# Kernel tuning notes

Measured on AMD Instinct MI355X. Metric: run time of the kernel, lower is better.

## Reference

```python
import jax, jax.numpy as jnp
import numpy as np

N, E, M = 4096, 65536, 16   # nodes, edges, channel multiplicity per degree
MID = 32                    # RadialFunc hidden width (SE3-Transformer default)
EPS = 1e-5                  # BatchNorm1d eps
DEGS = [0, 1]
PAIRS = [(0, 0), (0, 1), (1, 0), (1, 1)]  # (d_in, d_out)


def _bn_relu(x, g, b):
    # BatchNorm1d in training mode (biased batch stats over edges) + ReLU
    mu = x.mean(0, keepdims=True)
    var = ((x - mu) ** 2).mean(0, keepdims=True)
    return jax.nn.relu((x - mu) / jnp.sqrt(var + EPS) * g + b)


def _radial(feat, w1, b1, g1, be1, w2, b2, g2, be2, w3, b3, nf):
    # RadialFunc: Linear-BN-ReLU, Linear-BN-ReLU, Linear -> [E, nc_out, 1, nc_in, 1, nf]
    y = _bn_relu(feat @ w1 + b1, g1, be1)
    y = _bn_relu(y @ w2 + b2, g2, be2)
    y = y @ w3 + b3
    return y.reshape(-1, M, 1, M, 1, nf)


def _forward(h0, h1, r, basis00, basis01, basis10, basis11,
             rw1, rb1, rg1, rbe1, rw2, rb2, rg2, rbe2,
             w3_00, b3_00, w3_01, b3_01, w3_10, b3_10, w3_11, b3_11,
             Wself0, Wself1, edge_src, edge_dst):
    h = {0: h0, 1: h1}
    basis = {(0, 0): basis00, (0, 1): basis01, (1, 0): basis10, (1, 1): basis11}
    w3b3 = {(0, 0): (w3_00, b3_00), (0, 1): (w3_01, b3_01),
            (1, 0): (w3_10, b3_10), (1, 1): (w3_11, b3_11)}
    Wself = {0: Wself0, 1: Wself1}
    # PairwiseConv: per-edge kernel = sum_f R * basis  -> [E, M, 2do+1, M, 2di+1]
    kern = {}
    for p, (di, do) in enumerate(PAIRS):
        nf = 2 * min(di, do) + 1
        w3, b3 = w3b3[(di, do)]
        R = _radial(r, rw1[p], rb1[p], rg1[p], rbe1[p],
                    rw2[p], rb2[p], rg2[p], rbe2[p], w3, b3, nf)
        kern[(di, do)] = (R * basis[(di, do)]).sum(-1)
    cnt = jnp.maximum(
        jax.ops.segment_sum(jnp.ones((E,), h0.dtype), edge_dst, num_segments=N), 1.0)
    outs = []
    for do in DEGS:
        msg = jnp.zeros((E, M, 2 * do + 1), h0.dtype)
        for di in DEGS:
            # per-edge small matmul: kernel @ gathered source feature
            msg = msg + jnp.einsum('eopiq,eiq->eop', kern[(di, do)], h[di][edge_src])
        # self-interaction, flavor='skip': add W @ destination feature per edge
        msg = msg + jnp.einsum('mi,eip->emp', Wself[do][0], h[do][edge_dst])
        s = jax.ops.segment_sum(msg, edge_dst, num_segments=N)  # scatter-mean
        outs.append(s / cnt[:, None, None])
    return tuple(outs)


def setup_inputs() -> dict:
    key = jax.random.key(0)
    ks = jax.random.split(key, 20)
    nrm = lambda k, sh, s=1.0: jax.random.normal(k, sh, jnp.float32) * s
    return {
        'h0': nrm(ks[0], (N, M, 1)),
        'h1': nrm(ks[1], (N, M, 3)),
        'r': jax.random.uniform(ks[2], (E, 1), jnp.float32),
        'basis00': nrm(ks[3], (E, 1, 1, 1, 1, 1)),
        'basis01': nrm(ks[4], (E, 1, 3, 1, 1, 1)),
        'basis10': nrm(ks[5], (E, 1, 1, 1, 3, 1)),
        'basis11': nrm(ks[6], (E, 1, 3, 1, 3, 3)),
        'rw1': nrm(ks[7], (4, 1, MID)),
        'rb1': jnp.zeros((4, MID), jnp.float32),
        'rg1': jnp.ones((4, MID), jnp.float32),
        'rbe1': jnp.zeros((4, MID), jnp.float32),
        'rw2': nrm(ks[8], (4, MID, MID), 1.0 / np.sqrt(MID)),
        'rb2': jnp.zeros((4, MID), jnp.float32),
        'rg2': jnp.ones((4, MID), jnp.float32),
        'rbe2': jnp.zeros((4, MID), jnp.float32),
        'w3_00': nrm(ks[9], (MID, M * M), 1.0 / np.sqrt(MID)),
        'b3_00': jnp.zeros((M * M,), jnp.float32),
        'w3_01': nrm(ks[10], (MID, M * M), 1.0 / np.sqrt(MID)),
        'b3_01': jnp.zeros((M * M,), jnp.float32),
        'w3_10': nrm(ks[11], (MID, M * M), 1.0 / np.sqrt(MID)),
        'b3_10': jnp.zeros((M * M,), jnp.float32),
        'w3_11': nrm(ks[12], (MID, M * M * 3), 1.0 / np.sqrt(MID)),
        'b3_11': jnp.zeros((M * M * 3,), jnp.float32),
        'Wself0': nrm(ks[13], (1, M, M), 1.0 / np.sqrt(M)),
        'Wself1': nrm(ks[14], (1, M, M), 1.0 / np.sqrt(M)),
        'edge_src': jax.random.randint(ks[15], (E,), 0, N),
        'edge_dst': jax.random.randint(ks[16], (E,), 0, N),
    }


def reference(h0, h1, r, basis00, basis01, basis10, basis11,
              rw1, rb1, rg1, rbe1, rw2, rb2, rg2, rbe2,
              w3_00, b3_00, w3_01, b3_01, w3_10, b3_10, w3_11, b3_11,
              Wself0, Wself1, edge_src, edge_dst):
    return _forward(h0, h1, r, basis00, basis01, basis10, basis11,
                    rw1, rb1, rg1, rbe1, rw2, rb2, rg2, rbe2,
                    w3_00, b3_00, w3_01, b3_01, w3_10, b3_10, w3_11, b3_11,
                    Wself0, Wself1, edge_src, edge_dst)
```

## Files before the change

kernel.cpp:

```cpp
#include <hip/hip_runtime.h>

#define N_NODES 4096
#define N_EDGES 65536
#define MID 32
#define BN_EPS 1e-5f

#define WS_RSUM    0
#define WS_RSUMSQ  1
#define WS_ALPHA1  272
#define WS_BETA1   400
#define WS_A2      528
#define WS_S2      656
#define WS_GRAM    5120
#define WS_SUMY    9216
#define WS_W2T     17664
#define WS_MSG_F   262144
#define WS_U00     4456448
#define WS_U01     4521984
#define WS_V10     4587520
#define WS_W11     4784128
#define WS_DEG_I   1024
#define WS_CUR_I   9344
#define WS_OFFS_I  13440
#define WS_ELIST_I 65536
#define WSB_WA     524288
#define WSB_WB     557056
#define WSB_WC     573440

typedef short bf16x8 __attribute__((ext_vector_type(8)));
typedef float f32x4  __attribute__((ext_vector_type(4)));

__device__ __forceinline__ unsigned short f2bf(float x) {
    unsigned u = __float_as_uint(x);
    u += 0x7fffu + ((u >> 16) & 1u);
    return (unsigned short)(u >> 16);
}

__global__ void __launch_bounds__(256) k_pre(const float* __restrict__ rw2,
        const float* __restrict__ w300, const float* __restrict__ w301,
        const float* __restrict__ w310, const float* __restrict__ w311,
        const float* __restrict__ bw300, const float* __restrict__ bw301,
        const float* __restrict__ bw310, const float* __restrict__ bw311,
        const float* __restrict__ r, const int* __restrict__ edst,
        const float* __restrict__ h0, const float* __restrict__ h1,
        float* __restrict__ wsf) {
    if (blockIdx.x < 128) {
        int t = blockIdx.x * 256 + threadIdx.x;
        char* wsb = (char*)wsf;
        if (t < 4096) {
            int p = t >> 10, rem = t & 1023, c = rem >> 5, k = rem & 31;
            wsf[WS_W2T + t] = rw2[(p << 10) + (k << 5) + c];
        }
        if (t < 16384) {
            int col = t >> 5, k = t & 31;
            float v = (col < 256) ? w300[(k << 8) + col] : w310[(k << 8) + (col - 256)];
            ((unsigned short*)(wsb + WSB_WA))[t] = f2bf(v);
        }
        if (t < 8192) {
            int col = t >> 5, k = t & 31;
            ((unsigned short*)(wsb + WSB_WB))[t] = f2bf(w301[(k << 8) + col]);
        }
        if (t < 24576) {
            int col = t >> 5, k = t & 31;
            int f = col >> 8, rem = col & 255;
            ((unsigned short*)(wsb + WSB_WC))[t] = f2bf(w311[k * 768 + rem * 3 + f]);
        }
    } else if (blockIdx.x < 384) {
        int e = (blockIdx.x - 128) * 256 + threadIdx.x;
        float v = r[e];
        atomicAdd(((int*)wsf) + WS_DEG_I + edst[e], 1);
        float s = v, ss = v * v;
#pragma unroll
        for (int mk = 32; mk >= 1; mk >>= 1) {
            s  += __shfl_xor(s,  mk, 64);
            ss += __shfl_xor(ss, mk, 64);
        }
        __shared__ float ls[4], lss[4];
        int lane = threadIdx.x & 63, wv = threadIdx.x >> 6;
        if (lane == 0) { ls[wv] = s; lss[wv] = ss; }
        __syncthreads();
        if (threadIdx.x == 0) {
            atomicAdd(wsf + WS_RSUM,   ls[0] + ls[1] + ls[2] + ls[3]);
            atomicAdd(wsf + WS_RSUMSQ, lss[0] + lss[1] + lss[2] + lss[3]);
        }
    } else {
        int g = (blockIdx.x - 384) * 256 + threadIdx.x;
        int n = g >> 4, mo = g & 15;
        float s00 = 0.f, s01 = 0.f;
#pragma unroll
        for (int mi = 0; mi < 16; ++mi) {
            float hv = h0[n * 16 + mi];
            s00 += bw300[mo * 16 + mi] * hv;
            s01 += bw301[mo * 16 + mi] * hv;
        }
        wsf[WS_U00 + n * 16 + mo] = s00;
        wsf[WS_U01 + n * 16 + mo] = s01;
#pragma unroll
        for (int q = 0; q < 3; ++q) {
            float sv = 0.f;
#pragma unroll
            for (int mi = 0; mi < 16; ++mi)
                sv += bw310[mo * 16 + mi] * h1[n * 48 + mi * 3 + q];
            wsf[WS_V10 + n * 48 + q * 16 + mo] = sv;
        }
#pragma unroll 1
        for (int f = 0; f < 3; ++f)
#pragma unroll 1
            for (int q = 0; q < 3; ++q) {
                float sv = 0.f;
#pragma unroll
                for (int mi = 0; mi < 16; ++mi)
                    sv += bw311[(mo * 16 + mi) * 3 + f] * h1[n * 48 + mi * 3 + q];
                wsf[WS_W11 + n * 144 + (f * 3 + q) * 16 + mo] = sv;
            }
    }
}

__global__ void __launch_bounds__(512) k_gram(const float* __restrict__ r,
        const float* __restrict__ rw1, const float* __restrict__ rg1,
        const float* __restrict__ rbe1, float* __restrict__ wsf) {
    int t = threadIdx.x;
    int wv = t >> 6, lane = t & 63;
    int quad = lane >> 4, lq = lane & 15;
    int p  = __builtin_amdgcn_readfirstlane(wv & 3);
    int mt = __builtin_amdgcn_readfirstlane(wv >> 2);
    float mu_r  = wsf[WS_RSUM] * (1.f / N_EDGES);
    float var_r = wsf[WS_RSUMSQ] * (1.f / N_EDGES) - mu_r * mu_r;
    float al[2], be[2];
#pragma unroll
    for (int hh = 0; hh < 2; ++hh) {
        int ch = p * 32 + hh * 16 + lq;
        float w1 = rw1[ch];
        float a = w1 * rg1[ch] * rsqrtf(w1 * w1 * var_r + BN_EPS);
        al[hh] = a;
        be[hh] = rbe1[ch] - a * mu_r;
    }
    bf16x8 ones;
#pragma unroll
    for (int j = 0; j < 8; ++j) ones[j] = (short)0x3F80;
    f32x4 accG0 = {0.f, 0.f, 0.f, 0.f};
    f32x4 accG1 = {0.f, 0.f, 0.f, 0.f};
    f32x4 accS  = {0.f, 0.f, 0.f, 0.f};
    int ebase = blockIdx.x * 512;
#pragma unroll 1
    for (int ks = 0; ks < 16; ++ks) {
        const float* rp = r + ebase + ks * 32 + quad * 8;
        float4 ra = *(const float4*)(rp);
        float4 rb = *(const float4*)(rp + 4);
        float rv[8] = {ra.x, ra.y, ra.z, ra.w, rb.x, rb.y, rb.z, rb.w};
        bf16x8 fr0, fr1;
#pragma unroll
        for (int j = 0; j < 8; ++j) {
            fr0[j] = (short)f2bf(fmaxf(0.f, al[0] * rv[j] + be[0]));
            fr1[j] = (short)f2bf(fmaxf(0.f, al[1] * rv[j] + be[1]));
        }
        bf16x8 fA = mt ? fr1 : fr0;
        accG0 = __builtin_amdgcn_mfma_f32_16x16x32_bf16(fA, fr0, accG0, 0, 0, 0);
        accG1 = __builtin_amdgcn_mfma_f32_16x16x32_bf16(fA, fr1, accG1, 0, 0, 0);
        accS  = __builtin_amdgcn_mfma_f32_16x16x32_bf16(fA, ones, accS,  0, 0, 0);
    }
    float* G = wsf + WS_GRAM + p * 1024;
#pragma unroll
    for (int reg = 0; reg < 4; ++reg) {
        int k1 = mt * 16 + quad * 4 + reg;
        atomicAdd(&G[k1 * 32 + lq],      accG0[reg]);
        atomicAdd(&G[k1 * 32 + 16 + lq], accG1[reg]);
    }
    if (lq == 0) {
#pragma unroll
        for (int reg = 0; reg < 4; ++reg)
            atomicAdd(wsf + WS_SUMY + p * 32 + mt * 16 + quad * 4 + reg, accS[reg]);
    }
}

__global__ void __launch_bounds__(1024) k_fs(const float* __restrict__ rw1,
        const float* __restrict__ rg1, const float* __restrict__ rbe1,
        const float* __restrict__ rg2, const float* __restrict__ rbe2,
        const float* __restrict__ rb2, float* __restrict__ wsf) {
    int t = threadIdx.x;
    if (t < 128) {
        float mu_r  = wsf[WS_RSUM] * (1.f / N_EDGES);
        float var_r = wsf[WS_RSUMSQ] * (1.f / N_EDGES) - mu_r * mu_r;
        float w1 = rw1[t];
        float al = w1 * rg1[t] * rsqrtf(w1 * w1 * var_r + BN_EPS);
        wsf[WS_ALPHA1 + t] = al;
        wsf[WS_BETA1  + t] = rbe1[t] - al * mu_r;
        int p = t >> 5, c = t & 31;
        const float* G = wsf + WS_GRAM + p * 1024;
        const float* w = wsf + WS_W2T + p * 1024 + c * 32;
        float invE = 1.f / N_EDGES;
        float s1 = 0.f;
#pragma unroll 1
        for (int k = 0; k < 32; ++k) s1 += w[k] * (wsf[WS_SUMY + p * 32 + k] * invE);
        float q = 0.f;
#pragma unroll 1
        for (int k1 = 0; k1 < 32; ++k1) {
            float a = 0.f;
#pragma unroll
            for (int k2 = 0; k2 < 32; ++k2) a += w[k2] * G[k1 * 32 + k2];
            q += w[k1] * a;
        }
        float var = q * invE - s1 * s1;
        float a2 = rg2[t] * rsqrtf(var + BN_EPS);
        wsf[WS_A2 + t] = a2;
        float mu2 = rb2[t] + s1;
        wsf[WS_S2 + t] = rbe2[t] - mu2 * a2;
    }
    __shared__ int sdata[1024];
    const int* deg = ((const int*)wsf) + WS_DEG_I;
    int* offs = ((int*)wsf) + WS_OFFS_I;
    int* cur  = ((int*)wsf) + WS_CUR_I;
    int v0 = deg[t * 4], v1 = deg[t * 4 + 1], v2 = deg[t * 4 + 2], v3 = deg[t * 4 + 3];
    sdata[t] = v0 + v1 + v2 + v3;
    __syncthreads();
    for (int off = 1; off < 1024; off <<= 1) {
        int x = sdata[t];
        int y = (t >= off) ? sdata[t - off] : 0;
        __syncthreads();
        sdata[t] = x + y;
        __syncthreads();
    }
    int excl = (t == 0) ? 0 : sdata[t - 1];
    int o0 = excl, o1 = excl + v0, o2 = o1 + v1, o3 = o2 + v2;
    offs[t * 4] = o0;     cur[t * 4] = o0;
    offs[t * 4 + 1] = o1; cur[t * 4 + 1] = o1;
    offs[t * 4 + 2] = o2; cur[t * 4 + 2] = o2;
    offs[t * 4 + 3] = o3; cur[t * 4 + 3] = o3;
    if (t == 1023) offs[4096] = sdata[1023];
}

__global__ void __launch_bounds__(256) k_cb(const int* __restrict__ edst,
        const float* __restrict__ b00, const float* __restrict__ b01,
        const float* __restrict__ b10, const float* __restrict__ b11,
        const int* __restrict__ esrc, float* __restrict__ wsf,
        float* __restrict__ msg) {
    if (blockIdx.x < 256) {
        int e = blockIdx.x * 256 + threadIdx.x;
        int d = edst[e];
        int* cur   = ((int*)wsf) + WS_CUR_I;
        int* elist = ((int*)wsf) + WS_ELIST_I;
        int pos = atomicAdd(&cur[d], 1);
        elist[pos] = e;
        return;
    }
    int g = (blockIdx.x - 256) * 256 + threadIdx.x;
    int e = g >> 2, quad = g & 3;
    int s = esrc[e];
    float4 u00q = *(const float4*)(wsf + WS_U00 + s * 16 + quad * 4);
    float b00v = b00[e];
    float m0[4];
#pragma unroll
    for (int rr = 0; rr < 4; ++rr) m0[rr] = b00v * ((const float*)&u00q)[rr];
#pragma unroll
    for (int q = 0; q < 3; ++q) {
        float4 vq = *(const float4*)(wsf + WS_V10 + s * 48 + q * 16 + quad * 4);
        float bq = b10[e * 3 + q];
#pragma unroll
        for (int rr = 0; rr < 4; ++rr) m0[rr] += bq * ((const float*)&vq)[rr];
    }
    {
        float4 w = {m0[0], m0[1], m0[2], m0[3]};
        *(float4*)(msg + (size_t)e * 64 + quad * 4) = w;
    }
    float4 u01q = *(const float4*)(wsf + WS_U01 + s * 16 + quad * 4);
    float bo0 = b01[e * 3 + 0], bo1 = b01[e * 3 + 1], bo2 = b01[e * 3 + 2];
    float m1[4][3];
#pragma unroll
    for (int rr = 0; rr < 4; ++rr) {
        float u = ((const float*)&u01q)[rr];
        m1[rr][0] = bo0 * u; m1[rr][1] = bo1 * u; m1[rr][2] = bo2 * u;
    }
#pragma unroll
    for (int f = 0; f < 3; ++f)
#pragma unroll
        for (int q = 0; q < 3; ++q) {
            float4 wq = *(const float4*)(wsf + WS_W11 + s * 144 + (f * 3 + q) * 16 + quad * 4);
#pragma unroll
            for (int o = 0; o < 3; ++o) {
                float bas = b11[e * 27 + o * 9 + q * 3 + f];
#pragma unroll
                for (int rr = 0; rr < 4; ++rr) m1[rr][o] += bas * ((const float*)&wq)[rr];
            }
        }
    float* base = msg + (size_t)e * 64 + 16 + quad * 12;
    float4 w0 = {m1[0][0], m1[0][1], m1[0][2], m1[1][0]};
    float4 w1 = {m1[1][1], m1[1][2], m1[2][0], m1[2][1]};
    float4 w2 = {m1[2][2], m1[3][0], m1[3][1], m1[3][2]};
    *(float4*)(base)     = w0;
    *(float4*)(base + 4) = w1;
    *(float4*)(base + 8) = w2;
}

__device__ __forceinline__ void y2_lds16(int p, int el, int c0, float rv,
                                         const float* __restrict__ wsf,
                                         const float* __restrict__ rb2, char* dst) {
    float y1[MID];
#pragma unroll
    for (int k = 0; k < MID; ++k)
        y1[k] = fmaxf(0.f, wsf[WS_ALPHA1 + p * 32 + k] * rv + wsf[WS_BETA1 + p * 32 + k]);
    unsigned short h[16];
#pragma unroll
    for (int cc = 0; cc < 16; ++cc) {
        int c = c0 + cc;
        float x = rb2[p * 32 + c];
#pragma unroll
        for (int k = 0; k < MID; ++k) x += y1[k] * wsf[WS_W2T + p * 1024 + c * 32 + k];
        h[cc] = f2bf(fmaxf(0.f, wsf[WS_A2 + p * 32 + c] * x + wsf[WS_S2 + p * 32 + c]));
    }
#pragma unroll
    for (int q = 0; q < 2; ++q) {
        int4 pk;
        pk.x = (int)h[q * 8 + 0] | ((int)h[q * 8 + 1] << 16);
        pk.y = (int)h[q * 8 + 2] | ((int)h[q * 8 + 3] << 16);
        pk.z = (int)h[q * 8 + 4] | ((int)h[q * 8 + 5] << 16);
        pk.w = (int)h[q * 8 + 6] | ((int)h[q * 8 + 7] << 16);
        *(int4*)(dst + el * 64 + c0 * 2 + q * 16) = pk;
    }
}

__global__ void __launch_bounds__(512, 2) k_msg(const float* __restrict__ r,
        const float* __restrict__ h0, const float* __restrict__ h1,
        const float* __restrict__ b00, const float* __restrict__ b01,
        const float* __restrict__ b10, const float* __restrict__ b11,
        const float* __restrict__ rb2,
        const int* __restrict__ esrc,
        const float* __restrict__ wsf, float* __restrict__ msg) {
    extern __shared__ char smem[];
    short* w3s = (short*)smem;
    const char* wsb = (const char*)wsf;
    int t = threadIdx.x;
    int wv = t >> 6, lane = t & 63;
    int quad = lane >> 4, lq = lane & 15;
    int eb = blockIdx.x << 7;
    int el = wv * 16 + lq;
    int e = eb + el;

    {
        const float4* src = (const float4*)(wsb + WSB_WA);
        float4* dst = (float4*)smem;
#pragma unroll
        for (int i = 0; i < 4; ++i) dst[i * 512 + t] = src[i * 512 + t];
    }
    {
        int g = t >> 7;
        int p = __builtin_amdgcn_readfirstlane((g >> 1) * 2);
        int c0 = (g & 1) * 16;
        int el2 = t & 127;
        y2_lds16(p, el2, c0, r[eb + el2], wsf, rb2, smem + 32768 + (g >> 1) * 8192);
    }
    __syncthreads();
    {
        int s = esrc[e];
        bf16x8 bf0 = *(const bf16x8*)(smem + 32768 + el * 64 + quad * 16);
        bf16x8 bf2 = *(const bf16x8*)(smem + 40960 + el * 64 + quad * 16);
        float4 h0q = *(const float4*)(h0 + s * 16 + quad * 4);
        float4 hv0 = *(const float4*)(h1 + s * 48 + quad * 12);
        float4 hv1 = *(const float4*)(h1 + s * 48 + quad * 12 + 4);
        float4 hv2 = *(const float4*)(h1 + s * 48 + quad * 12 + 8);
        float b00v = b00[e];
        float bq0 = b10[e * 3 + 0], bq1 = b10[e * 3 + 1], bq2 = b10[e * 3 + 2];
        float gq0 = bq0 * hv0.x + bq1 * hv0.y + bq2 * hv0.z;
        float gq1 = bq0 * hv0.w + bq1 * hv1.x + bq2 * hv1.y;
        float gq2 = bq0 * hv1.z + bq1 * hv1.w + bq2 * hv2.x;
        float gq3 = bq0 * hv2.y + bq1 * hv2.z + bq2 * hv2.w;
        float4 a0v = *(const float4*)(msg + (size_t)e * 64 + quad * 4);
        float a0[4] = {a0v.x, a0v.y, a0v.z, a0v.w};
#pragma unroll
        for (int m = 0; m < 16; ++m) {
            bf16x8 af = *(const bf16x8*)(w3s + (m * 16 + lq) * 32 + quad * 8);
            f32x4 dd = __builtin_amdgcn_mfma_f32_16x16x32_bf16(af, bf0, (f32x4){0.f,0.f,0.f,0.f}, 0, 0, 0);
            float partial = dd[0] * h0q.x + dd[1] * h0q.y + dd[2] * h0q.z + dd[3] * h0q.w;
            partial += __shfl_xor(partial, 16);
            partial += __shfl_xor(partial, 32);
            a0[m & 3] += (quad == (m >> 2)) ? b00v * partial : 0.f;
        }
#pragma unroll
        for (int m = 0; m < 16; ++m) {
            bf16x8 af = *(const bf16x8*)(w3s + ((256 + m * 16 + lq) << 5) + quad * 8);
            f32x4 dd = __builtin_amdgcn_mfma_f32_16x16x32_bf16(af, bf2, (f32x4){0.f,0.f,0.f,0.f}, 0, 0, 0);
            float partial = dd[0] * gq0 + dd[1] * gq1 + dd[2] * gq2 + dd[3] * gq3;
            partial += __shfl_xor(partial, 16);
            partial += __shfl_xor(partial, 32);
            a0[m & 3] += (quad == (m >> 2)) ? partial : 0.f;
        }
        float4 w = {a0[0], a0[1], a0[2], a0[3]};
        *(float4*)(msg + (size_t)e * 64 + quad * 4) = w;
    }
    __syncthreads();

    {
        const float4* src = (const float4*)(wsb + WSB_WB);
        float4* dst = (float4*)smem;
#pragma unroll
        for (int i = 0; i < 2; ++i) dst[i * 512 + t] = src[i * 512 + t];
    }
    if (t < 256) {
        int el2 = t & 127, c0 = (t >> 7) * 16;
        y2_lds16(1, el2, c0, r[eb + el2], wsf, rb2, smem + 16384);
    }
    __syncthreads();
    {
        int s = esrc[e];
        bf16x8 bf1 = *(const bf16x8*)(smem + 16384 + el * 64 + quad * 16);
        float4 h0q = *(const float4*)(h0 + s * 16 + quad * 4);
        float d1[4] = {0.f, 0.f, 0.f, 0.f};
#pragma unroll
        for (int m = 0; m < 16; ++m) {
            bf16x8 af = *(const bf16x8*)(w3s + (m * 16 + lq) * 32 + quad * 8);
            f32x4 dd = __builtin_amdgcn_mfma_f32_16x16x32_bf16(af, bf1, (f32x4){0.f,0.f,0.f,0.f}, 0, 0, 0);
            float partial = dd[0] * h0q.x + dd[1] * h0q.y + dd[2] * h0q.z + dd[3] * h0q.w;
            partial += __shfl_xor(partial, 16);
            partial += __shfl_xor(partial, 32);
            d1[m & 3] += (quad == (m >> 2)) ? partial : 0.f;
        }
        float bo0 = b01[e * 3 + 0], bo1 = b01[e * 3 + 1], bo2 = b01[e * 3 + 2];
        float* base = msg + (size_t)e * 64 + 16 + quad * 12;
        float4 r0 = *(const float4*)(base);
        float4 r1 = *(const float4*)(base + 4);
        float4 r2 = *(const float4*)(base + 8);
        float4 w0 = {r0.x + bo0 * d1[0], r0.y + bo1 * d1[0], r0.z + bo2 * d1[0], r0.w + bo0 * d1[1]};
        float4 w1 = {r1.x + bo1 * d1[1], r1.y + bo2 * d1[1], r1.z + bo0 * d1[2], r1.w + bo1 * d1[2]};
        float4 w2 = {r2.x + bo2 * d1[2], r2.y + bo0 * d1[3], r2.z + bo1 * d1[3], r2.w + bo2 * d1[3]};
        *(float4*)(base)     = w0;
        *(float4*)(base + 4) = w1;
        *(float4*)(base + 8) = w2;
    }
    __syncthreads();

    {
        const float4* src = (const float4*)(wsb + WSB_WC);
        float4* dst = (float4*)smem;
#pragma unroll
        for (int i = 0; i < 6; ++i) dst[i * 512 + t] = src[i * 512 + t];
    }
    if (t < 256) {
        int el2 = t & 127, c0 = (t >> 7) * 16;
        y2_lds16(3, el2, c0, r[eb + el2], wsf, rb2, smem + 49152);
    }
    __syncthreads();
    {
        int s = esrc[e];
        bf16x8 bf3 = *(const bf16x8*)(smem + 49152 + el * 64 + quad * 16);
        float4 hv0 = *(const float4*)(h1 + s * 48 + quad * 12);
        float4 hv1 = *(const float4*)(h1 + s * 48 + quad * 12 + 4);
        float4 hv2 = *(const float4*)(h1 + s * 48 + quad * 12 + 8);
        float h1v[4][3] = {{hv0.x, hv0.y, hv0.z}, {hv0.w, hv1.x, hv1.y},
                           {hv1.z, hv1.w, hv2.x}, {hv2.y, hv2.z, hv2.w}};
        float m1[4][3];
#pragma unroll
        for (int rr = 0; rr < 4; ++rr)
#pragma unroll
            for (int o = 0; o < 3; ++o) m1[rr][o] = 0.f;
#pragma unroll
        for (int f = 0; f < 3; ++f) {
            float Tf[4][3];
#pragma unroll
            for (int o = 0; o < 3; ++o) {
                float bv0 = b11[e * 27 + o * 9 + 0 + f];
                float bv1 = b11[e * 27 + o * 9 + 3 + f];
                float bv2 = b11[e * 27 + o * 9 + 6 + f];
#pragma unroll
                for (int rr = 0; rr < 4; ++rr)
                    Tf[rr][o] = h1v[rr][0] * bv0 + h1v[rr][1] * bv1 + h1v[rr][2] * bv2;
            }
#pragma unroll
            for (int m = 0; m < 16; ++m) {
                int colb = f * 256 + m * 16 + lq;
                bf16x8 af = *(const bf16x8*)(w3s + colb * 32 + quad * 8);
                f32x4 dd = __builtin_amdgcn_mfma_f32_16x16x32_bf16(af, bf3, (f32x4){0.f,0.f,0.f,0.f}, 0, 0, 0);
#pragma unroll
                for (int o = 0; o < 3; ++o) {
                    float po = dd[0] * Tf[0][o] + dd[1] * Tf[1][o] + dd[2] * Tf[2][o] + dd[3] * Tf[3][o];
                    po += __shfl_xor(po, 16);
                    po += __shfl_xor(po, 32);
                    m1[m & 3][o] += (quad == (m >> 2)) ? po : 0.f;
                }
            }
        }
        float* base = msg + (size_t)e * 64 + 16 + quad * 12;
        float4 r0 = *(const float4*)(base);
        float4 r1 = *(const float4*)(base + 4);
        float4 r2 = *(const float4*)(base + 8);
        float4 w0 = {m1[0][0] + r0.x, m1[0][1] + r0.y, m1[0][2] + r0.z, m1[1][0] + r0.w};
        float4 w1 = {m1[1][1] + r1.x, m1[1][2] + r1.y, m1[2][0] + r1.z, m1[2][1] + r1.w};
        float4 w2 = {m1[2][2] + r2.x, m1[3][0] + r2.y, m1[3][1] + r2.z, m1[3][2] + r2.w};
        *(float4*)(base)     = w0;
        *(float4*)(base + 4) = w1;
        *(float4*)(base + 8) = w2;
    }
}

__global__ void __launch_bounds__(256) k_gather(const float* __restrict__ h0,
        const float* __restrict__ h1, const float* __restrict__ Wself0,
        const float* __restrict__ Wself1, const float* __restrict__ wsf,
        float* __restrict__ out) {
    int wv = threadIdx.x >> 6, lane = threadIdx.x & 63;
    int n = blockIdx.x * 4 + wv;
    const int* offs  = ((const int*)wsf) + WS_OFFS_I;
    const int* elist = ((const int*)wsf) + WS_ELIST_I;
    const float* msg = wsf + WS_MSG_F;
    int start = offs[n], end = offs[n + 1];
    int deg = end - start;
    float acc = 0.f;
    for (int j0 = 0; j0 < deg; j0 += 64) {
        int cnt = min(64, deg - j0);
        int eidv = (j0 + lane < deg) ? elist[start + j0 + lane] : 0;
        int jj = 0;
        for (; jj + 3 < cnt; jj += 4) {
            int e0 = __shfl(eidv, jj), e1 = __shfl(eidv, jj + 1);
            int e2 = __shfl(eidv, jj + 2), e3 = __shfl(eidv, jj + 3);
            float v0 = msg[(size_t)e0 * 64 + lane];
            float v1 = msg[(size_t)e1 * 64 + lane];
            float v2 = msg[(size_t)e2 * 64 + lane];
            float v3 = msg[(size_t)e3 * 64 + lane];
            acc += (v0 + v1) + (v2 + v3);
        }
        for (; jj < cnt; ++jj) {
            int eid = __shfl(eidv, jj);
            acc += msg[(size_t)eid * 64 + lane];
        }
    }
    float self = 0.f;
    if (lane < 16) {
        int m = lane;
#pragma unroll
        for (int i = 0; i < 16; ++i) self += Wself0[m * 16 + i] * h0[n * 16 + i];
    } else {
        int idx = lane - 16; int m = idx / 3, o = idx % 3;
#pragma unroll
        for (int i = 0; i < 16; ++i) self += Wself1[m * 16 + i] * h1[n * 48 + i * 3 + o];
    }
    float c = (float)(deg > 0 ? deg : 1);
    float res = acc / c + (deg > 0 ? self : 0.f);
    if (lane < 16) out[n * 16 + lane] = res;
    else           out[65536 + n * 48 + (lane - 16)] = res;
}

extern "C" void kernel_launch(void* const* d_in, const int* in_sizes, int n_in,
                              void* d_out, int out_size, void* d_ws, size_t ws_size,
                              hipStream_t stream) {
    const float* h0   = (const float*)d_in[0];
    const float* h1   = (const float*)d_in[1];
    const float* r    = (const float*)d_in[2];
    const float* b00  = (const float*)d_in[3];
    const float* b01  = (const float*)d_in[4];
    const float* b10  = (const float*)d_in[5];
    const float* b11  = (const float*)d_in[6];
    const float* rw1  = (const float*)d_in[7];
    const float* rg1  = (const float*)d_in[9];
    const float* rbe1 = (const float*)d_in[10];
    const float* rw2  = (const float*)d_in[11];
    const float* rb2  = (const float*)d_in[12];
    const float* rg2  = (const float*)d_in[13];
    const float* rbe2 = (const float*)d_in[14];
    const float* w300 = (const float*)d_in[15];
    const float* bw300= (const float*)d_in[16];
    const float* w301 = (const float*)d_in[17];
    const float* bw301= (const float*)d_in[18];
    const float* w310 = (const float*)d_in[19];
    const float* bw310= (const float*)d_in[20];
    const float* w311 = (const float*)d_in[21];
    const float* bw311= (const float*)d_in[22];
    const float* Wself0 = (const float*)d_in[23];
    const float* Wself1 = (const float*)d_in[24];
    const int* esrc = (const int*)d_in[25];
    const int* edst = (const int*)d_in[26];
    float* out = (float*)d_out;
    float* wsf = (float*)d_ws;
    float* msg = wsf + WS_MSG_F;

    static bool attr_set = false;
    if (!attr_set) {
        hipFuncSetAttribute((const void*)k_msg,
                            hipFuncAttributeMaxDynamicSharedMemorySize, 57344);
        attr_set = true;
    }

    hipMemsetAsync(d_ws, 0, 37376, stream);

    k_pre<<<640, 256, 0, stream>>>(rw2, w300, w301, w310, w311,
                                   bw300, bw301, bw310, bw311, r, edst, h0, h1, wsf);
    k_gram<<<128, 512, 0, stream>>>(r, rw1, rg1, rbe1, wsf);
    k_fs<<<1, 1024, 0, stream>>>(rw1, rg1, rbe1, rg2, rbe2, rb2, wsf);
    k_cb<<<1280, 256, 0, stream>>>(edst, b00, b01, b10, b11, esrc, wsf, msg);
    k_msg<<<512, 512, 57344, stream>>>(r, h0, h1, b00, b01, b10, b11, rb2,
                                       esrc, wsf, msg);
    k_gather<<<1024, 256, 0, stream>>>(h0, h1, Wself0, Wself1, wsf, out);
}
```

Baseline: 269.8 us.

## Process 256 edges per k_msg block and compute all radial hiddens upfront

```diff
diff --git a/kernel.cpp b/kernel.cpp
--- a/kernel.cpp
+++ b/kernel.cpp
@@ -86,6 +86,9 @@
     } else {
         int g = (blockIdx.x - 384) * 256 + threadIdx.x;
         int n = g >> 4, mo = g & 15;
+        float h1r[48];
+#pragma unroll
+        for (int j = 0; j < 48; ++j) h1r[j] = h1[n * 48 + j];
         float s00 = 0.f, s01 = 0.f;
 #pragma unroll
         for (int mi = 0; mi < 16; ++mi) {
@@ -100,17 +103,17 @@
             float sv = 0.f;
 #pragma unroll
             for (int mi = 0; mi < 16; ++mi)
-                sv += bw310[mo * 16 + mi] * h1[n * 48 + mi * 3 + q];
+                sv += bw310[mo * 16 + mi] * h1r[mi * 3 + q];
             wsf[WS_V10 + n * 48 + q * 16 + mo] = sv;
         }
-#pragma unroll 1
+#pragma unroll
         for (int f = 0; f < 3; ++f)
-#pragma unroll 1
+#pragma unroll
             for (int q = 0; q < 3; ++q) {
                 float sv = 0.f;
 #pragma unroll
                 for (int mi = 0; mi < 16; ++mi)
-                    sv += bw311[(mo * 16 + mi) * 3 + f] * h1[n * 48 + mi * 3 + q];
+                    sv += bw311[(mo * 16 + mi) * 3 + f] * h1r[mi * 3 + q];
                 wsf[WS_W11 + n * 144 + (f * 3 + q) * 16 + mo] = sv;
             }
     }
@@ -318,7 +321,7 @@
     }
 }
 
-__global__ void __launch_bounds__(512, 2) k_msg(const float* __restrict__ r,
+__global__ void __launch_bounds__(512) k_msg(const float* __restrict__ r,
         const float* __restrict__ h0, const float* __restrict__ h1,
         const float* __restrict__ b00, const float* __restrict__ b01,
         const float* __restrict__ b10, const float* __restrict__ b11,
@@ -331,28 +334,31 @@
     int t = threadIdx.x;
     int wv = t >> 6, lane = t & 63;
     int quad = lane >> 4, lq = lane & 15;
-    int eb = blockIdx.x << 7;
-    int el = wv * 16 + lq;
-    int e = eb + el;
+    int eb = blockIdx.x << 8;
 
     {
         const float4* src = (const float4*)(wsb + WSB_WA);
         float4* dst = (float4*)smem;
 #pragma unroll
-        for (int i = 0; i < 4; ++i) dst[i * 512 + t] = src[i * 512 + t];
+        for (int i = 0; i < 6; ++i) dst[i * 512 + t] = src[i * 512 + t];
     }
     {
-        int g = t >> 7;
-        int p = __builtin_amdgcn_readfirstlane((g >> 1) * 2);
-        int c0 = (g & 1) * 16;
-        int el2 = t & 127;
-        y2_lds16(p, el2, c0, r[eb + el2], wsf, rb2, smem + 32768 + (g >> 1) * 8192);
+        int el2 = t & 255, c0 = ((t >> 8) & 1) * 16;
+        float rv = r[eb + el2];
+        y2_lds16(0, el2, c0, rv, wsf, rb2, smem + 49152);
+        y2_lds16(1, el2, c0, rv, wsf, rb2, smem + 49152 + 16384);
+        y2_lds16(2, el2, c0, rv, wsf, rb2, smem + 49152 + 32768);
+        y2_lds16(3, el2, c0, rv, wsf, rb2, smem + 49152 + 49152);
     }
     __syncthreads();
-    {
+
+#pragma unroll 1
+    for (int g2 = 0; g2 < 2; ++g2) {
+        int el = g2 * 128 + wv * 16 + lq;
+        int e = eb + el;
         int s = esrc[e];
-        bf16x8 bf0 = *(const bf16x8*)(smem + 32768 + el * 64 + quad * 16);
-        bf16x8 bf2 = *(const bf16x8*)(smem + 40960 + el * 64 + quad * 16);
+        bf16x8 bf0 = *(const bf16x8*)(smem + 49152 + el * 64 + quad * 16);
+        bf16x8 bf2 = *(const bf16x8*)(smem + 49152 + 32768 + el * 64 + quad * 16);
         float4 h0q = *(const float4*)(h0 + s * 16 + quad * 4);
         float4 hv0 = *(const float4*)(h1 + s * 48 + quad * 12);
         float4 hv1 = *(const float4*)(h1 + s * 48 + quad * 12 + 4);
@@ -383,30 +389,15 @@
             partial += __shfl_xor(partial, 32);
             a0[m & 3] += (quad == (m >> 2)) ? partial : 0.f;
         }
-        float4 w = {a0[0], a0[1], a0[2], a0[3]};
-        *(float4*)(msg + (size_t)e * 64 + quad * 4) = w;
-    }
-    __syncthreads();
-
-    {
-        const float4* src = (const float4*)(wsb + WSB_WB);
-        float4* dst = (float4*)smem;
-#pragma unroll
-        for (int i = 0; i < 2; ++i) dst[i * 512 + t] = src[i * 512 + t];
-    }
-    if (t < 256) {
-        int el2 = t & 127, c0 = (t >> 7) * 16;
-        y2_lds16(1, el2, c0, r[eb + el2], wsf, rb2, smem + 16384);
-    }
-    __syncthreads();
-    {
-        int s = esrc[e];
-        bf16x8 bf1 = *(const bf16x8*)(smem + 16384 + el * 64 + quad * 16);
-        float4 h0q = *(const float4*)(h0 + s * 16 + quad * 4);
+        {
+            float4 w = {a0[0], a0[1], a0[2], a0[3]};
+            *(float4*)(msg + (size_t)e * 64 + quad * 4) = w;
+        }
+        bf16x8 bf1 = *(const bf16x8*)(smem + 49152 + 16384 + el * 64 + quad * 16);
         float d1[4] = {0.f, 0.f, 0.f, 0.f};
 #pragma unroll
         for (int m = 0; m < 16; ++m) {
-            bf16x8 af = *(const bf16x8*)(w3s + (m * 16 + lq) * 32 + quad * 8);
+            bf16x8 af = *(const bf16x8*)(w3s + ((512 + m * 16 + lq) << 5) + quad * 8);
             f32x4 dd = __builtin_amdgcn_mfma_f32_16x16x32_bf16(af, bf1, (f32x4){0.f,0.f,0.f,0.f}, 0, 0, 0);
             float partial = dd[0] * h0q.x + dd[1] * h0q.y + dd[2] * h0q.z + dd[3] * h0q.w;
             partial += __shfl_xor(partial, 16);
@@ -433,14 +424,14 @@
 #pragma unroll
         for (int i = 0; i < 6; ++i) dst[i * 512 + t] = src[i * 512 + t];
     }
-    if (t < 256) {
-        int el2 = t & 127, c0 = (t >> 7) * 16;
-        y2_lds16(3, el2, c0, r[eb + el2], wsf, rb2, smem + 49152);
-    }
     __syncthreads();
-    {
+
+#pragma unroll 1
+    for (int g2 = 0; g2 < 2; ++g2) {
+        int el = g2 * 128 + wv * 16 + lq;
+        int e = eb + el;
         int s = esrc[e];
-        bf16x8 bf3 = *(const bf16x8*)(smem + 49152 + el * 64 + quad * 16);
+        bf16x8 bf3 = *(const bf16x8*)(smem + 49152 + 49152 + el * 64 + quad * 16);
         float4 hv0 = *(const float4*)(h1 + s * 48 + quad * 12);
         float4 hv1 = *(const float4*)(h1 + s * 48 + quad * 12 + 4);
         float4 hv2 = *(const float4*)(h1 + s * 48 + quad * 12 + 8);
@@ -572,7 +563,7 @@
     static bool attr_set = false;
     if (!attr_set) {
         hipFuncSetAttribute((const void*)k_msg,
-                            hipFuncAttributeMaxDynamicSharedMemorySize, 57344);
+                            hipFuncAttributeMaxDynamicSharedMemorySize, 114688);
         attr_set = true;
     }
 
@@ -583,7 +574,7 @@
     k_gram<<<128, 512, 0, stream>>>(r, rw1, rg1, rbe1, wsf);
     k_fs<<<1, 1024, 0, stream>>>(rw1, rg1, rbe1, rg2, rbe2, rb2, wsf);
     k_cb<<<1280, 256, 0, stream>>>(edst, b00, b01, b10, b11, esrc, wsf, msg);
-    k_msg<<<512, 512, 57344, stream>>>(r, h0, h1, b00, b01, b10, b11, rb2,
-                                       esrc, wsf, msg);
+    k_msg<<<256, 512, 114688, stream>>>(r, h0, h1, b00, b01, b10, b11, rb2,
+                                        esrc, wsf, msg);
     k_gather<<<1024, 256, 0, stream>>>(h0, h1, Wself0, Wself1, wsf, out);
 }
```

After: 317.3 us. 1.18x slower.

## Process 256 edges per k_msg block to amortize weight staging; cache h1 in registers

Applied to the files above, without the earlier changes.

```diff
diff --git a/kernel.cpp b/kernel.cpp
--- a/kernel.cpp
+++ b/kernel.cpp
@@ -86,6 +86,9 @@
     } else {
         int g = (blockIdx.x - 384) * 256 + threadIdx.x;
         int n = g >> 4, mo = g & 15;
+        float h1r[48];
+#pragma unroll
+        for (int j = 0; j < 48; ++j) h1r[j] = h1[n * 48 + j];
         float s00 = 0.f, s01 = 0.f;
 #pragma unroll
         for (int mi = 0; mi < 16; ++mi) {
@@ -100,17 +103,17 @@
             float sv = 0.f;
 #pragma unroll
             for (int mi = 0; mi < 16; ++mi)
-                sv += bw310[mo * 16 + mi] * h1[n * 48 + mi * 3 + q];
+                sv += bw310[mo * 16 + mi] * h1r[mi * 3 + q];
             wsf[WS_V10 + n * 48 + q * 16 + mo] = sv;
         }
-#pragma unroll 1
+#pragma unroll
         for (int f = 0; f < 3; ++f)
-#pragma unroll 1
+#pragma unroll
             for (int q = 0; q < 3; ++q) {
                 float sv = 0.f;
 #pragma unroll
                 for (int mi = 0; mi < 16; ++mi)
-                    sv += bw311[(mo * 16 + mi) * 3 + f] * h1[n * 48 + mi * 3 + q];
+                    sv += bw311[(mo * 16 + mi) * 3 + f] * h1r[mi * 3 + q];
                 wsf[WS_W11 + n * 144 + (f * 3 + q) * 16 + mo] = sv;
             }
     }
@@ -331,9 +334,7 @@
     int t = threadIdx.x;
     int wv = t >> 6, lane = t & 63;
     int quad = lane >> 4, lq = lane & 15;
-    int eb = blockIdx.x << 7;
-    int el = wv * 16 + lq;
-    int e = eb + el;
+    int eb = blockIdx.x << 8;
 
     {
         const float4* src = (const float4*)(wsb + WSB_WA);
@@ -342,17 +343,21 @@
         for (int i = 0; i < 4; ++i) dst[i * 512 + t] = src[i * 512 + t];
     }
     {
-        int g = t >> 7;
-        int p = __builtin_amdgcn_readfirstlane((g >> 1) * 2);
-        int c0 = (g & 1) * 16;
-        int el2 = t & 127;
-        y2_lds16(p, el2, c0, r[eb + el2], wsf, rb2, smem + 32768 + (g >> 1) * 8192);
+        int p = __builtin_amdgcn_readfirstlane((t >> 8) * 2);
+        int el = t & 255;
+        float rv = r[eb + el];
+        char* dst = smem + 32768 + (t >> 8) * 16384;
+        y2_lds16(p, el, 0, rv, wsf, rb2, dst);
+        y2_lds16(p, el, 16, rv, wsf, rb2, dst);
     }
     __syncthreads();
-    {
+#pragma unroll
+    for (int g2 = 0; g2 < 2; ++g2) {
+        int el = (wv * 2 + g2) * 16 + lq;
+        int e = eb + el;
         int s = esrc[e];
         bf16x8 bf0 = *(const bf16x8*)(smem + 32768 + el * 64 + quad * 16);
-        bf16x8 bf2 = *(const bf16x8*)(smem + 40960 + el * 64 + quad * 16);
+        bf16x8 bf2 = *(const bf16x8*)(smem + 49152 + el * 64 + quad * 16);
         float4 h0q = *(const float4*)(h0 + s * 16 + quad * 4);
         float4 hv0 = *(const float4*)(h1 + s * 48 + quad * 12);
         float4 hv1 = *(const float4*)(h1 + s * 48 + quad * 12 + 4);
@@ -394,12 +399,15 @@
 #pragma unroll
         for (int i = 0; i < 2; ++i) dst[i * 512 + t] = src[i * 512 + t];
     }
-    if (t < 256) {
-        int el2 = t & 127, c0 = (t >> 7) * 16;
-        y2_lds16(1, el2, c0, r[eb + el2], wsf, rb2, smem + 16384);
+    {
+        int el = t & 255, c0 = (t >> 8) * 16;
+        y2_lds16(1, el, c0, r[eb + el], wsf, rb2, smem + 16384);
     }
     __syncthreads();
-    {
+#pragma unroll
+    for (int g2 = 0; g2 < 2; ++g2) {
+        int el = (wv * 2 + g2) * 16 + lq;
+        int e = eb + el;
         int s = esrc[e];
         bf16x8 bf1 = *(const bf16x8*)(smem + 16384 + el * 64 + quad * 16);
         float4 h0q = *(const float4*)(h0 + s * 16 + quad * 4);
@@ -433,12 +441,15 @@
 #pragma unroll
         for (int i = 0; i < 6; ++i) dst[i * 512 + t] = src[i * 512 + t];
     }
-    if (t < 256) {
-        int el2 = t & 127, c0 = (t >> 7) * 16;
-        y2_lds16(3, el2, c0, r[eb + el2], wsf, rb2, smem + 49152);
+    {
+        int el = t & 255, c0 = (t >> 8) * 16;
+        y2_lds16(3, el, c0, r[eb + el], wsf, rb2, smem + 49152);
     }
     __syncthreads();
-    {
+#pragma unroll
+    for (int g2 = 0; g2 < 2; ++g2) {
+        int el = (wv * 2 + g2) * 16 + lq;
+        int e = eb + el;
         int s = esrc[e];
         bf16x8 bf3 = *(const bf16x8*)(smem + 49152 + el * 64 + quad * 16);
         float4 hv0 = *(const float4*)(h1 + s * 48 + quad * 12);
@@ -572,7 +583,7 @@
     static bool attr_set = false;
     if (!attr_set) {
         hipFuncSetAttribute((const void*)k_msg,
-                            hipFuncAttributeMaxDynamicSharedMemorySize, 57344);
+                            hipFuncAttributeMaxDynamicSharedMemorySize, 65536);
         attr_set = true;
     }
 
@@ -583,7 +594,7 @@
     k_gram<<<128, 512, 0, stream>>>(r, rw1, rg1, rbe1, wsf);
     k_fs<<<1, 1024, 0, stream>>>(rw1, rg1, rbe1, rg2, rbe2, rb2, wsf);
     k_cb<<<1280, 256, 0, stream>>>(edst, b00, b01, b10, b11, esrc, wsf, msg);
-    k_msg<<<512, 512, 57344, stream>>>(r, h0, h1, b00, b01, b10, b11, rb2,
+    k_msg<<<256, 512, 65536, stream>>>(r, h0, h1, b00, b01, b10, b11, rb2,
                                        esrc, wsf, msg);
     k_gather<<<1024, 256, 0, stream>>>(h0, h1, Wself0, Wself1, wsf, out);
 }
```

New measurement: 250.6 us. -7.1%, faster.
